# Optimization experiments

Hardware: AMD Instinct MI355X
Metric: run time of the kernel (lower is better)

The kernel has to match this reference:

```python
import math
import jax, jax.numpy as jnp
import numpy as np

B, T, C, H = 2, 2048, 1024, 16
MAX_SEQ = 2048


def _make_pe(max_seq: int, dim: int, base: float = 10000.0) -> np.ndarray:
    pe = np.zeros((max_seq, dim), dtype=np.float32)
    position = np.arange(max_seq, dtype=np.float32)[:, None]
    div_term = np.exp(np.arange(0, dim, 2, dtype=np.float32) * (-math.log(base) / dim))
    pe[:, 0::2] = np.sin(position * div_term)
    pe[:, 1::2] = np.cos(position * div_term)
    return pe


def setup_inputs() -> dict:
    key = jax.random.key(0)
    k1, k2, k3 = jax.random.split(key, 3)
    x = jax.random.normal(k1, (B, T, C), dtype=jnp.float32)
    # torch Linear default init scale ~ 1/sqrt(fan_in)
    w_qkv = jax.random.normal(k2, (3 * C, C), dtype=jnp.float32) / math.sqrt(C)
    w_proj = jax.random.normal(k3, (C, C), dtype=jnp.float32) / math.sqrt(C)
    pe = jnp.asarray(_make_pe(MAX_SEQ, C))
    return {"x": x, "w_qkv": w_qkv, "w_proj": w_proj, "pe": pe}


def reference(x, w_qkv, w_proj, pe):
    b, t, c = x.shape
    h = H
    d = c // h
    # RoPE module adds sinusoidal PE under torch.no_grad() -> stop_gradient
    xp = jax.lax.stop_gradient(x + pe[None, :t, :])
    qkv = xp @ w_qkv.T  # [b, t, 3c]
    q, k, v = jnp.split(qkv, 3, axis=-1)
    q = q.reshape(b, t, h, d).transpose(0, 2, 1, 3)  # bhtd
    k = k.reshape(b, t, h, d).transpose(0, 2, 1, 3)
    v = v.reshape(b, t, h, d).transpose(0, 2, 1, 3)
    att = jnp.einsum("bhqd,bhkd->bhqk", q, k) * (1.0 / math.sqrt(d))
    causal = jnp.tril(jnp.ones((t, t), dtype=bool))  # [t, t]
    att = jnp.where(causal[None, None], att, -jnp.inf)
    att = jax.nn.softmax(att, axis=-1)
    y = jnp.einsum("bhqk,bhkd->bhqd", att, v)
    y = y.transpose(0, 2, 1, 3).reshape(b, t, c)
    return y @ w_proj.T
```

## Files before the change

kernel.cpp:

```cpp
#include <hip/hip_runtime.h>
#include <cstdint>

typedef __bf16 bf16x8 __attribute__((ext_vector_type(8)));
typedef __bf16 bf16x4 __attribute__((ext_vector_type(4)));
typedef float  f32x4  __attribute__((ext_vector_type(4)));

static constexpr int kB = 2, kT = 2048, kC = 1024, kH = 16, kD = 64;
static constexpr int kK = 1024;

__device__ __forceinline__ uint16_t f2bf(float f) {
  uint32_t u = __builtin_bit_cast(uint32_t, f);
  u += 0x7FFFu + ((u >> 16) & 1u);
  return (uint16_t)(u >> 16);
}

__device__ __forceinline__ void gl_lds16(const void* g, void* l) {
  __builtin_amdgcn_global_load_lds((__attribute__((address_space(1))) void*)(void*)g,
                                   (__attribute__((address_space(3))) void*)l, 16, 0, 0);
}

__global__ __launch_bounds__(256) void prep_all(const float* __restrict__ x,
                                                const float* __restrict__ pe,
                                                const float* __restrict__ wqkv,
                                                const float* __restrict__ wproj,
                                                uint16_t* __restrict__ xp,
                                                uint16_t* __restrict__ wq,
                                                uint16_t* __restrict__ wp) {
  constexpr int NX = kB * kT * kC / 4;
  constexpr int NWQ = 3 * kC * kC / 4;
  const int i = blockIdx.x * 256 + threadIdx.x;
  if (i < NX) {
    const float4 xv = ((const float4*)x)[i];
    const int c4 = i & (kC / 4 - 1);
    const int t = (i / (kC / 4)) & (kT - 1);
    const float4 pv = ((const float4*)pe)[t * (kC / 4) + c4];
    ushort4 o;
    o.x = f2bf(xv.x + pv.x);
    o.y = f2bf(xv.y + pv.y);
    o.z = f2bf(xv.z + pv.z);
    o.w = f2bf(xv.w + pv.w);
    ((ushort4*)xp)[i] = o;
  } else if (i < NX + NWQ) {
    const int j = i - NX;
    const float4 v = ((const float4*)wqkv)[j];
    ushort4 u;
    u.x = f2bf(v.x); u.y = f2bf(v.y); u.z = f2bf(v.z); u.w = f2bf(v.w);
    ((ushort4*)wq)[j] = u;
  } else {
    const int j = i - NX - NWQ;
    const float4 v = ((const float4*)wproj)[j];
    ushort4 u;
    u.x = f2bf(v.x); u.y = f2bf(v.y); u.z = f2bf(v.z); u.w = f2bf(v.w);
    ((ushort4*)wp)[j] = u;
  }
}

__global__ __launch_bounds__(512, 2) void gemm_qkv(const uint16_t* __restrict__ A,
                                                   const uint16_t* __restrict__ W,
                                                   uint16_t* __restrict__ qb,
                                                   uint16_t* __restrict__ kb,
                                                   uint16_t* __restrict__ vT) {
  __shared__ __align__(1024) char lds[131072];
  const int tid = threadIdx.x;
  const int lane = tid & 63;
  const int wid = tid >> 6;
  const int l15 = lane & 15, l4 = lane >> 4;
  const int WM = wid >> 2, WN = wid & 3;
  const int orig = (int)blockIdx.x;
  const int xcd = orig & 7, j = orig >> 3;
  const int m0 = (xcd * 2 + (j & 1)) * 256;
  const int n0 = (j >> 1) * 256;

  f32x4 acc[2][4][4] = {};
  bf16x8 bfp[2][4];

  auto stage = [&](int isA, int buf, int kt) {
#pragma unroll
    for (int c = 0; c < 4; ++c) {
      const int off = (c * 512 + tid) * 16;
      const int lr = off >> 7, cbl = off & 127;
      const size_t grow = (size_t)((isA ? m0 : n0) + lr) * kK + kt * 64;
      gl_lds16((const char*)(isA ? A : W) + grow * 2 + (cbl ^ ((lr & 7) << 4)),
               lds + (isA ? 0 : 65536) + buf * 32768 + off);
    }
  };

#define QKV_PHASE(CBUF, H, SA, SBUF, KT, VM)                                      \
  {                                                                               \
    stage(SA, SBUF, KT);                                                          \
    if (VM == 4)                                                                  \
      asm volatile("s_waitcnt vmcnt(4)" ::: "memory");                            \
    else                                                                          \
      asm volatile("s_waitcnt vmcnt(8)" ::: "memory");                            \
    __builtin_amdgcn_s_barrier();                                                 \
    asm volatile("" ::: "memory");                                                \
    const char* Ab = lds + (CBUF)*32768;                                          \
    const char* Bb = lds + 65536 + (CBUF)*32768;                                  \
    if ((H) == 0) {                                                               \
      _Pragma("unroll") for (int ks = 0; ks < 2; ++ks)                            \
          _Pragma("unroll") for (int nt = 0; nt < 4; ++nt) {                      \
        const int lr = WN * 64 + nt * 16 + l15;                                   \
        bfp[ks][nt] = *(const bf16x8*)(Bb + lr * 128 +                            \
                                       ((ks * 64 + l4 * 16) ^ ((lr & 7) << 4)));  \
      }                                                                           \
    }                                                                             \
    _Pragma("unroll") for (int ks = 0; ks < 2; ++ks) {                            \
      bf16x8 af[4];                                                               \
      _Pragma("unroll") for (int mt = 0; mt < 4; ++mt) {                          \
        const int lr = (H)*128 + WM * 64 + mt * 16 + l15;                         \
        af[mt] = *(const bf16x8*)(Ab + lr * 128 +                                 \
                                  ((ks * 64 + l4 * 16) ^ ((lr & 7) << 4)));       \
      }                                                                           \
      __builtin_amdgcn_s_setprio(1);                                              \
      _Pragma("unroll") for (int mt = 0; mt < 4; ++mt)                            \
          _Pragma("unroll") for (int nt = 0; nt < 4; ++nt)                        \
              acc[H][mt][nt] = __builtin_amdgcn_mfma_f32_16x16x32_bf16(           \
                  af[mt], bfp[ks][nt], acc[H][mt][nt], 0, 0, 0);                  \
      __builtin_amdgcn_s_setprio(0);                                              \
    }                                                                             \
    asm volatile("" ::: "memory");                                                \
    __builtin_amdgcn_s_barrier();                                                 \
    asm volatile("" ::: "memory");                                                \
  }

  stage(1, 0, 0);
  stage(0, 0, 0);

  for (int i = 0; i < 8; ++i) {
    const int ktb1 = 2 * i + 1;
    const int ktb0 = (2 * i + 2 > 15) ? 15 : 2 * i + 2;
    QKV_PHASE(0, 0, 1, 1, ktb1, 4);
    QKV_PHASE(0, 1, 0, 1, ktb1, 8);
    QKV_PHASE(1, 0, 1, 0, ktb0, 4);
    QKV_PHASE(1, 1, 0, 0, ktb0, 8);
  }
  asm volatile("s_waitcnt vmcnt(0)" ::: "memory");
  __builtin_amdgcn_s_barrier();
  asm volatile("" ::: "memory");

  const int sec = n0 >> 10;
  const int b = m0 >> 11, tb = m0 & (kT - 1);
  if (sec < 2) {
    uint16_t* dst = (sec == 0) ? qb : kb;
#pragma unroll
    for (int h = 0; h < 2; ++h)
#pragma unroll
      for (int mt = 0; mt < 4; ++mt)
#pragma unroll
        for (int nt = 0; nt < 4; ++nt)
#pragma unroll
          for (int r = 0; r < 4; ++r) {
            const int m = h * 128 + WM * 64 + mt * 16 + l4 * 4 + r;
            const int nn = (n0 & (kC - 1)) + WN * 64 + nt * 16 + l15;
            const int hh = nn >> 6, d = nn & 63;
            dst[((size_t)((b * kH + hh) * kT + tb + m)) * kD + d] =
                f2bf(acc[h][mt][nt][r]);
          }
  } else {
#pragma unroll
    for (int h = 0; h < 2; ++h)
#pragma unroll
      for (int mt = 0; mt < 4; ++mt)
#pragma unroll
        for (int nt = 0; nt < 4; ++nt) {
          const int nl = WN * 64 + nt * 16 + l15;
          const int mb2 = (h * 128 + WM * 64 + mt * 16 + l4 * 4) * 2;
          ushort4 pk;
          pk.x = f2bf(acc[h][mt][nt][0]);
          pk.y = f2bf(acc[h][mt][nt][1]);
          pk.z = f2bf(acc[h][mt][nt][2]);
          pk.w = f2bf(acc[h][mt][nt][3]);
          *(ushort4*)(lds + nl * 512 + (mb2 ^ ((nl & 7) << 4))) = pk;
        }
    asm volatile("" ::: "memory");
    __builtin_amdgcn_s_barrier();
    asm volatile("" ::: "memory");
#pragma unroll
    for (int it = 0; it < 16; ++it) {
      const int chunk = it * 512 + tid;
      const int nr = chunk >> 5, mb = (chunk & 31) * 16;
      const bf16x8 v = *(const bf16x8*)(lds + nr * 512 + (mb ^ ((nr & 7) << 4)));
      const int nn = (n0 - 2048) + nr;
      const int hh = nn >> 6, d = nn & 63;
      *(bf16x8*)(vT + ((size_t)((b * kH + hh) * kD + d)) * kT + tb + (chunk & 31) * 8) = v;
    }
  }
#undef QKV_PHASE
}

__global__ __launch_bounds__(256) void gemm_proj(const uint16_t* __restrict__ A,
                                                 const uint16_t* __restrict__ W,
                                                 float* __restrict__ out) {
  __shared__ __align__(1024) char lds[32768];
  const int lane = threadIdx.x & 63;
  const int wid = threadIdx.x >> 6;
  const int l15 = lane & 15, l4 = lane >> 4;
  const int wm = wid >> 1, wn = wid & 1;
  const int orig = (int)(blockIdx.y * gridDim.x + blockIdx.x);
  const int xcd = orig & 7, j = orig >> 3;
  const int m0 = (xcd * 4 + (j & 3)) * 128;
  const int n0 = (j >> 2) * 128;

  f32x4 acc[4][4] = {};

  for (int k0 = 0; k0 < kK; k0 += 64) {
#pragma unroll
    for (int jj = 0; jj < 4; ++jj) {
      const int off = wid * 4096 + jj * 1024 + lane * 16;
      const int row = off >> 7;
      const int colb = (off & 127) ^ ((row & 7) << 4);
      gl_lds16((const char*)A + ((size_t)(m0 + row) * kK + k0) * 2 + colb,
               lds + wid * 4096 + jj * 1024);
      gl_lds16((const char*)W + ((size_t)(n0 + row) * kK + k0) * 2 + colb,
               lds + 16384 + wid * 4096 + jj * 1024);
    }
    __syncthreads();
#pragma unroll
    for (int ks = 0; ks < 2; ++ks) {
      bf16x8 af[4], bf_[4];
#pragma unroll
      for (int mt = 0; mt < 4; ++mt) {
        const int r = wm * 64 + mt * 16 + l15;
        const int cb = (l4 * 16 + ks * 64) ^ ((r & 7) << 4);
        af[mt] = *(const bf16x8*)(lds + r * 128 + cb);
      }
#pragma unroll
      for (int nt = 0; nt < 4; ++nt) {
        const int r = wn * 64 + nt * 16 + l15;
        const int cb = (l4 * 16 + ks * 64) ^ ((r & 7) << 4);
        bf_[nt] = *(const bf16x8*)(lds + 16384 + r * 128 + cb);
      }
#pragma unroll
      for (int mt = 0; mt < 4; ++mt)
#pragma unroll
        for (int nt = 0; nt < 4; ++nt)
          acc[mt][nt] = __builtin_amdgcn_mfma_f32_16x16x32_bf16(af[mt], bf_[nt],
                                                                acc[mt][nt], 0, 0, 0);
    }
    __syncthreads();
  }

#pragma unroll
  for (int mt = 0; mt < 4; ++mt)
#pragma unroll
    for (int nt = 0; nt < 4; ++nt)
#pragma unroll
      for (int r = 0; r < 4; ++r) {
        const int m = m0 + wm * 64 + mt * 16 + l4 * 4 + r;
        const int n = n0 + wn * 64 + nt * 16 + l15;
        out[(size_t)m * kC + n] = acc[mt][nt][r];
      }
}

__global__ __launch_bounds__(256, 4) void attn(const uint16_t* __restrict__ qb,
                                               const uint16_t* __restrict__ kb,
                                               const uint16_t* __restrict__ vT,
                                               uint16_t* __restrict__ y) {
  __shared__ __align__(1024) char lds[40960];
  const int lane = threadIdx.x & 63;
  const int wid = threadIdx.x >> 6;
  const int l15 = lane & 15, l4 = lane >> 4;
  const int bh = blockIdx.x;
  const int qt = (int)(gridDim.y - 1) - (int)blockIdx.y;
  const int q0 = qt * 64 + wid * 16;
  const size_t base = (size_t)bh * kT * kD;
  const uint16_t* Q = qb + base;
  const uint16_t* Kp = kb + base;
  const uint16_t* Vt = vT + base;
  char* P = lds + 32768 + wid * 2048;
  const int xr = (l15 & 7) << 4;

  bf16x8 qf[2];
#pragma unroll
  for (int ks = 0; ks < 2; ++ks) {
    bf16x8 t = *(const bf16x8*)(Q + (size_t)(q0 + l15) * kD + ks * 32 + l4 * 8);
#pragma unroll
    for (int i = 0; i < 8; ++i) t[i] = (__bf16)((float)t[i] * 0.1803368801f);
    qf[ks] = t;
  }
  bf16x8 ones;
#pragma unroll
  for (int i = 0; i < 8; ++i) ones[i] = (__bf16)1.0f;

  float m_ = -1e30f;
  f32x4 o[4];
  f32x4 ol = {0.f, 0.f, 0.f, 0.f};
#pragma unroll
  for (int nt = 0; nt < 4; ++nt) o[nt] = (f32x4){0.f, 0.f, 0.f, 0.f};

  const int nkt = qt + 1;

  auto STAGE = [&](int bi, int k0) {
#pragma unroll
    for (int c = 0; c < 2; ++c) {
      const int call = wid * 2 + c;
      const int row = call * 8 + (lane >> 3);
      const int colb = (((lane & 7) ^ ((lane >> 3) & 7)) << 4);
      gl_lds16((const char*)Kp + ((size_t)(k0 + row) * kD) * 2 + colb,
               lds + bi * 8192 + call * 1024);
      gl_lds16((const char*)Vt + ((size_t)row * kT + k0) * 2 + colb,
               lds + 16384 + bi * 8192 + call * 1024);
    }
  };

  int cur = 0;
  STAGE(0, 0);
  for (int kt = 0; kt < nkt; ++kt) {
    const int k0 = kt * 64;
    const bool hasnext = (kt + 1 < nkt);
    if (hasnext) STAGE(cur ^ 1, k0 + 64);
    if (hasnext)
      asm volatile("s_waitcnt vmcnt(4)" ::: "memory");
    else
      asm volatile("s_waitcnt vmcnt(0)" ::: "memory");
    __builtin_amdgcn_s_barrier();
    asm volatile("" ::: "memory");

    const char* Kb = lds + cur * 8192;
    const char* Vb = lds + 16384 + cur * 8192;

    f32x4 s[4] = {};
    __builtin_amdgcn_s_setprio(1);
#pragma unroll
    for (int ks = 0; ks < 2; ++ks)
#pragma unroll
      for (int nt = 0; nt < 4; ++nt) {
        const bf16x8 kf =
            *(const bf16x8*)(Kb + (nt * 16 + l15) * 128 + ((ks * 64 + l4 * 16) ^ xr));
        s[nt] = __builtin_amdgcn_mfma_f32_16x16x32_bf16(kf, qf[ks], s[nt], 0, 0, 0);
      }
    __builtin_amdgcn_s_setprio(0);

    if (kt == nkt - 1) {
      const int qq = q0 + l15;
#pragma unroll
      for (int nt = 0; nt < 4; ++nt)
#pragma unroll
        for (int r = 0; r < 4; ++r)
          if (k0 + nt * 16 + l4 * 4 + r > qq) s[nt][r] = -1e30f;
    }

    float pm = s[0][0];
#pragma unroll
    for (int nt = 0; nt < 4; ++nt)
#pragma unroll
      for (int r = 0; r < 4; ++r) pm = fmaxf(pm, s[nt][r]);
    if (!__all(pm <= m_ + 11.0f)) {
      float rm = fmaxf(pm, __shfl_xor(pm, 16));
      rm = fmaxf(rm, __shfl_xor(rm, 32));
      const float newm = fmaxf(m_, rm);
      const float sc = exp2f(m_ - newm);
      m_ = newm;
#pragma unroll
      for (int nt = 0; nt < 4; ++nt)
#pragma unroll
        for (int r = 0; r < 4; ++r) o[nt][r] *= sc;
#pragma unroll
      for (int r = 0; r < 4; ++r) ol[r] *= sc;
    }
#pragma unroll
    for (int nt = 0; nt < 4; ++nt)
#pragma unroll
      for (int r = 0; r < 4; ++r) s[nt][r] = exp2f(s[nt][r] - m_);

#pragma unroll
    for (int nt = 0; nt < 4; ++nt) {
      bf16x4 pk;
#pragma unroll
      for (int r = 0; r < 4; ++r) pk[r] = (__bf16)s[nt][r];
      *(bf16x4*)(P + l15 * 128 + ((nt * 32 + l4 * 8) ^ xr)) = pk;
    }
    asm volatile("s_waitcnt lgkmcnt(0)" ::: "memory");
    __builtin_amdgcn_sched_barrier(0);

    bf16x8 pf[2];
#pragma unroll
    for (int ks = 0; ks < 2; ++ks)
      pf[ks] = *(const bf16x8*)(P + l15 * 128 + ((ks * 64 + l4 * 16) ^ xr));
    __builtin_amdgcn_s_setprio(1);
#pragma unroll
    for (int ks = 0; ks < 2; ++ks) {
#pragma unroll
      for (int nt = 0; nt < 4; ++nt) {
        const bf16x8 vf =
            *(const bf16x8*)(Vb + (nt * 16 + l15) * 128 + ((ks * 64 + l4 * 16) ^ xr));
        o[nt] = __builtin_amdgcn_mfma_f32_16x16x32_bf16(vf, pf[ks], o[nt], 0, 0, 0);
      }
      ol = __builtin_amdgcn_mfma_f32_16x16x32_bf16(ones, pf[ks], ol, 0, 0, 0);
    }
    __builtin_amdgcn_s_setprio(0);

    __builtin_amdgcn_s_barrier();
    asm volatile("" ::: "memory");
    cur ^= 1;
  }

  const float inv = 1.0f / ol[0];
  const int b = bh >> 4, h = bh & 15;
  const int q = q0 + l15;
#pragma unroll
  for (int nt = 0; nt < 4; ++nt) {
    bf16x4 yv;
#pragma unroll
    for (int r = 0; r < 4; ++r) yv[r] = (__bf16)(o[nt][r] * inv);
    *(bf16x4*)(y + ((size_t)(b * kT + q)) * kC + h * kD + nt * 16 + l4 * 4) = yv;
  }
}

extern "C" void kernel_launch(void* const* d_in, const int* in_sizes, int n_in,
                              void* d_out, int out_size, void* d_ws, size_t ws_size,
                              hipStream_t stream) {
  const float* x = (const float*)d_in[0];
  const float* wqkv = (const float*)d_in[1];
  const float* wproj = (const float*)d_in[2];
  const float* pe = (const float*)d_in[3];

  char* ws = (char*)d_ws;
  uint16_t* xp = (uint16_t*)(ws);
  uint16_t* wq = (uint16_t*)(ws + (size_t)(8u << 20));
  uint16_t* wp = (uint16_t*)(ws + (size_t)(14u << 20));
  uint16_t* qbuf = (uint16_t*)(ws + (size_t)(16u << 20));
  uint16_t* kbuf = (uint16_t*)(ws + (size_t)(24u << 20));
  uint16_t* vTb = (uint16_t*)(ws + (size_t)(32u << 20));

  prep_all<<<dim3(8192), 256, 0, stream>>>(x, pe, wqkv, wproj, xp, wq, wp);

  gemm_qkv<<<dim3(192), 512, 0, stream>>>(xp, wq, qbuf, kbuf, vTb);

  attn<<<dim3(kB * kH, kT / 64), 256, 0, stream>>>(qbuf, kbuf, vTb, xp);

  gemm_proj<<<dim3(32, 8), 256, 0, stream>>>(xp, wp, (float*)d_out);
}
```

Baseline: 108.0 us.

## Retile QKV GEMM to 256x192 for full CU occupancy; pipeline projection GEMM

The QKV GEMM changes from 256x256 to 256x192 tiles, so the grid grows from 192 to 256 blocks and fills all 256 CUs. Because a 192-wide tile can straddle the Q/K/V sections, the epilogue now picks the destination per element and writes vT with scattered strided stores, dropping the LDS transpose path. The projection GEMM is rewritten to use the same double-buffered, split-phase pipelined structure with waitcnt-based overlap. The risks are poorer coalescing of the vT stores and higher register use in the new proj kernel.

Measured after the change: 113.9 us. 5.5% more time.

```diff
diff --git a/kernel.cpp b/kernel.cpp
--- a/kernel.cpp
+++ b/kernel.cpp
@@ -60,7 +60,7 @@
                                                    uint16_t* __restrict__ qb,
                                                    uint16_t* __restrict__ kb,
                                                    uint16_t* __restrict__ vT) {
-  __shared__ __align__(1024) char lds[131072];
+  __shared__ __align__(1024) char lds[114688];
   const int tid = threadIdx.x;
   const int lane = tid & 63;
   const int wid = tid >> 6;
@@ -69,37 +69,47 @@
   const int orig = (int)blockIdx.x;
   const int xcd = orig & 7, j = orig >> 3;
   const int m0 = (xcd * 2 + (j & 1)) * 256;
-  const int n0 = (j >> 1) * 256;
-
-  f32x4 acc[2][4][4] = {};
-  bf16x8 bfp[2][4];
-
-  auto stage = [&](int isA, int buf, int kt) {
+  const int n0 = (j >> 1) * 192;
+
+  f32x4 acc[2][4][3] = {};
+  bf16x8 bfp[2][3];
+
+  auto stageA = [&](int buf, int kt) {
 #pragma unroll
     for (int c = 0; c < 4; ++c) {
       const int off = (c * 512 + tid) * 16;
       const int lr = off >> 7, cbl = off & 127;
-      const size_t grow = (size_t)((isA ? m0 : n0) + lr) * kK + kt * 64;
-      gl_lds16((const char*)(isA ? A : W) + grow * 2 + (cbl ^ ((lr & 7) << 4)),
-               lds + (isA ? 0 : 65536) + buf * 32768 + off);
+      gl_lds16((const char*)A + ((size_t)(m0 + lr) * kK + kt * 64) * 2 +
+                   (cbl ^ ((lr & 7) << 4)),
+               lds + buf * 32768 + off);
+    }
+  };
+  auto stageB = [&](int buf, int kt) {
+#pragma unroll
+    for (int c = 0; c < 3; ++c) {
+      const int off = (c * 512 + tid) * 16;
+      const int lr = off >> 7, cbl = off & 127;
+      gl_lds16((const char*)W + ((size_t)(n0 + lr) * kK + kt * 64) * 2 +
+                   (cbl ^ ((lr & 7) << 4)),
+               lds + 65536 + buf * 24576 + off);
     }
   };
 
 #define QKV_PHASE(CBUF, H, SA, SBUF, KT, VM)                                      \
   {                                                                               \
-    stage(SA, SBUF, KT);                                                          \
+    if (SA) stageA(SBUF, KT); else stageB(SBUF, KT);                              \
     if (VM == 4)                                                                  \
       asm volatile("s_waitcnt vmcnt(4)" ::: "memory");                            \
     else                                                                          \
-      asm volatile("s_waitcnt vmcnt(8)" ::: "memory");                            \
+      asm volatile("s_waitcnt vmcnt(7)" ::: "memory");                            \
     __builtin_amdgcn_s_barrier();                                                 \
     asm volatile("" ::: "memory");                                                \
     const char* Ab = lds + (CBUF)*32768;                                          \
-    const char* Bb = lds + 65536 + (CBUF)*32768;                                  \
+    const char* Bb = lds + 65536 + (CBUF)*24576;                                  \
     if ((H) == 0) {                                                               \
       _Pragma("unroll") for (int ks = 0; ks < 2; ++ks)                            \
-          _Pragma("unroll") for (int nt = 0; nt < 4; ++nt) {                      \
-        const int lr = WN * 64 + nt * 16 + l15;                                   \
+          _Pragma("unroll") for (int nt = 0; nt < 3; ++nt) {                      \
+        const int lr = WN * 48 + nt * 16 + l15;                                   \
         bfp[ks][nt] = *(const bf16x8*)(Bb + lr * 128 +                            \
                                        ((ks * 64 + l4 * 16) ^ ((lr & 7) << 4)));  \
       }                                                                           \
@@ -113,6 +123,112 @@
       }                                                                           \
       __builtin_amdgcn_s_setprio(1);                                              \
       _Pragma("unroll") for (int mt = 0; mt < 4; ++mt)                            \
+          _Pragma("unroll") for (int nt = 0; nt < 3; ++nt)                        \
+              acc[H][mt][nt] = __builtin_amdgcn_mfma_f32_16x16x32_bf16(           \
+                  af[mt], bfp[ks][nt], acc[H][mt][nt], 0, 0, 0);                  \
+      __builtin_amdgcn_s_setprio(0);                                              \
+    }                                                                             \
+    asm volatile("" ::: "memory");                                                \
+    __builtin_amdgcn_s_barrier();                                                 \
+    asm volatile("" ::: "memory");                                                \
+  }
+
+  stageA(0, 0);
+  stageB(0, 0);
+
+  for (int i = 0; i < 8; ++i) {
+    const int ktb1 = 2 * i + 1;
+    const int ktb0 = (2 * i + 2 > 15) ? 15 : 2 * i + 2;
+    QKV_PHASE(0, 0, 1, 1, ktb1, 4);
+    QKV_PHASE(0, 1, 0, 1, ktb1, 7);
+    QKV_PHASE(1, 0, 1, 0, ktb0, 4);
+    QKV_PHASE(1, 1, 0, 0, ktb0, 7);
+  }
+  asm volatile("s_waitcnt vmcnt(0)" ::: "memory");
+  __builtin_amdgcn_s_barrier();
+  asm volatile("" ::: "memory");
+
+  const int b = m0 >> 11, tb = m0 & (kT - 1);
+#pragma unroll
+  for (int h = 0; h < 2; ++h)
+#pragma unroll
+    for (int mt = 0; mt < 4; ++mt)
+#pragma unroll
+      for (int nt = 0; nt < 3; ++nt)
+#pragma unroll
+        for (int r = 0; r < 4; ++r) {
+          const int m = h * 128 + WM * 64 + mt * 16 + l4 * 4 + r;
+          const int t = tb + m;
+          const int n = n0 + WN * 48 + nt * 16 + l15;
+          const int sec = n >> 10, nn = n & (kC - 1);
+          const int hh = nn >> 6, d = nn & 63;
+          const uint16_t v = f2bf(acc[h][mt][nt][r]);
+          if (sec == 0)
+            qb[((size_t)((b * kH + hh) * kT + t)) * kD + d] = v;
+          else if (sec == 1)
+            kb[((size_t)((b * kH + hh) * kT + t)) * kD + d] = v;
+          else
+            vT[((size_t)((b * kH + hh) * kD + d)) * kT + t] = v;
+        }
+#undef QKV_PHASE
+}
+
+__global__ __launch_bounds__(256, 2) void gemm_proj(const uint16_t* __restrict__ A,
+                                                    const uint16_t* __restrict__ W,
+                                                    float* __restrict__ out) {
+  __shared__ __align__(1024) char lds[65536];
+  const int tid = threadIdx.x;
+  const int lane = tid & 63;
+  const int wid = tid >> 6;
+  const int l15 = lane & 15, l4 = lane >> 4;
+  const int WM = wid >> 1, WN = wid & 1;
+  const int orig = (int)blockIdx.x;
+  const int xcd = orig & 7, j = orig >> 3;
+  const int m0 = (xcd * 4 + (j & 3)) * 128;
+  const int n0 = (j >> 2) * 128;
+
+  f32x4 acc[2][2][4] = {};
+  bf16x8 bfp[2][4];
+
+  auto stage = [&](int isA, int buf, int kt) {
+#pragma unroll
+    for (int c = 0; c < 4; ++c) {
+      const int off = (c * 256 + tid) * 16;
+      const int lr = off >> 7, cbl = off & 127;
+      const size_t grow = (size_t)((isA ? m0 : n0) + lr) * kK + kt * 64;
+      gl_lds16((const char*)(isA ? A : W) + grow * 2 + (cbl ^ ((lr & 7) << 4)),
+               lds + (isA ? 0 : 32768) + buf * 16384 + off);
+    }
+  };
+
+#define PRJ_PHASE(CBUF, H, SA, SBUF, KT, VM)                                      \
+  {                                                                               \
+    stage(SA, SBUF, KT);                                                          \
+    if (VM == 4)                                                                  \
+      asm volatile("s_waitcnt vmcnt(4)" ::: "memory");                            \
+    else                                                                          \
+      asm volatile("s_waitcnt vmcnt(8)" ::: "memory");                            \
+    __builtin_amdgcn_s_barrier();                                                 \
+    asm volatile("" ::: "memory");                                                \
+    const char* Ab = lds + (CBUF)*16384;                                          \
+    const char* Bb = lds + 32768 + (CBUF)*16384;                                  \
+    if ((H) == 0) {                                                               \
+      _Pragma("unroll") for (int ks = 0; ks < 2; ++ks)                            \
+          _Pragma("unroll") for (int nt = 0; nt < 4; ++nt) {                      \
+        const int lr = WN * 64 + nt * 16 + l15;                                   \
+        bfp[ks][nt] = *(const bf16x8*)(Bb + lr * 128 +                            \
+                                       ((ks * 64 + l4 * 16) ^ ((lr & 7) << 4)));  \
+      }                                                                           \
+    }                                                                             \
+    _Pragma("unroll") for (int ks = 0; ks < 2; ++ks) {                            \
+      bf16x8 af[2];                                                               \
+      _Pragma("unroll") for (int mt = 0; mt < 2; ++mt) {                          \
+        const int lr = (H)*64 + WM * 32 + mt * 16 + l15;                          \
+        af[mt] = *(const bf16x8*)(Ab + lr * 128 +                                 \
+                                  ((ks * 64 + l4 * 16) ^ ((lr & 7) << 4)));       \
+      }                                                                           \
+      __builtin_amdgcn_s_setprio(1);                                              \
+      _Pragma("unroll") for (int mt = 0; mt < 2; ++mt)                            \
           _Pragma("unroll") for (int nt = 0; nt < 4; ++nt)                        \
               acc[H][mt][nt] = __builtin_amdgcn_mfma_f32_16x16x32_bf16(           \
                   af[mt], bfp[ks][nt], acc[H][mt][nt], 0, 0, 0);                  \
@@ -129,127 +245,28 @@
   for (int i = 0; i < 8; ++i) {
     const int ktb1 = 2 * i + 1;
     const int ktb0 = (2 * i + 2 > 15) ? 15 : 2 * i + 2;
-    QKV_PHASE(0, 0, 1, 1, ktb1, 4);
-    QKV_PHASE(0, 1, 0, 1, ktb1, 8);
-    QKV_PHASE(1, 0, 1, 0, ktb0, 4);
-    QKV_PHASE(1, 1, 0, 0, ktb0, 8);
+    PRJ_PHASE(0, 0, 1, 1, ktb1, 4);
+    PRJ_PHASE(0, 1, 0, 1, ktb1, 8);
+    PRJ_PHASE(1, 0, 1, 0, ktb0, 4);
+    PRJ_PHASE(1, 1, 0, 0, ktb0, 8);
   }
   asm volatile("s_waitcnt vmcnt(0)" ::: "memory");
   __builtin_amdgcn_s_barrier();
   asm volatile("" ::: "memory");
 
-  const int sec = n0 >> 10;
-  const int b = m0 >> 11, tb = m0 & (kT - 1);
-  if (sec < 2) {
-    uint16_t* dst = (sec == 0) ? qb : kb;
-#pragma unroll
-    for (int h = 0; h < 2; ++h)
-#pragma unroll
-      for (int mt = 0; mt < 4; ++mt)
-#pragma unroll
-        for (int nt = 0; nt < 4; ++nt)
-#pragma unroll
-          for (int r = 0; r < 4; ++r) {
-            const int m = h * 128 + WM * 64 + mt * 16 + l4 * 4 + r;
-            const int nn = (n0 & (kC - 1)) + WN * 64 + nt * 16 + l15;
-            const int hh = nn >> 6, d = nn & 63;
-            dst[((size_t)((b * kH + hh) * kT + tb + m)) * kD + d] =
-                f2bf(acc[h][mt][nt][r]);
-          }
-  } else {
-#pragma unroll
-    for (int h = 0; h < 2; ++h)
-#pragma unroll
-      for (int mt = 0; mt < 4; ++mt)
-#pragma unroll
-        for (int nt = 0; nt < 4; ++nt) {
-          const int nl = WN * 64 + nt * 16 + l15;
-          const int mb2 = (h * 128 + WM * 64 + mt * 16 + l4 * 4) * 2;
-          ushort4 pk;
-          pk.x = f2bf(acc[h][mt][nt][0]);
-          pk.y = f2bf(acc[h][mt][nt][1]);
-          pk.z = f2bf(acc[h][mt][nt][2]);
-          pk.w = f2bf(acc[h][mt][nt][3]);
-          *(ushort4*)(lds + nl * 512 + (mb2 ^ ((nl & 7) << 4))) = pk;
+#pragma unroll
+  for (int h = 0; h < 2; ++h)
+#pragma unroll
+    for (int mt = 0; mt < 2; ++mt)
+#pragma unroll
+      for (int nt = 0; nt < 4; ++nt)
+#pragma unroll
+        for (int r = 0; r < 4; ++r) {
+          const int m = m0 + h * 64 + WM * 32 + mt * 16 + l4 * 4 + r;
+          const int n = n0 + WN * 64 + nt * 16 + l15;
+          out[(size_t)m * kC + n] = acc[h][mt][nt][r];
         }
-    asm volatile("" ::: "memory");
-    __builtin_amdgcn_s_barrier();
-    asm volatile("" ::: "memory");
-#pragma unroll
-    for (int it = 0; it < 16; ++it) {
-      const int chunk = it * 512 + tid;
-      const int nr = chunk >> 5, mb = (chunk & 31) * 16;
-      const bf16x8 v = *(const bf16x8*)(lds + nr * 512 + (mb ^ ((nr & 7) << 4)));
-      const int nn = (n0 - 2048) + nr;
-      const int hh = nn >> 6, d = nn & 63;
-      *(bf16x8*)(vT + ((size_t)((b * kH + hh) * kD + d)) * kT + tb + (chunk & 31) * 8) = v;
-    }
-  }
-#undef QKV_PHASE
-}
-
-__global__ __launch_bounds__(256) void gemm_proj(const uint16_t* __restrict__ A,
-                                                 const uint16_t* __restrict__ W,
-                                                 float* __restrict__ out) {
-  __shared__ __align__(1024) char lds[32768];
-  const int lane = threadIdx.x & 63;
-  const int wid = threadIdx.x >> 6;
-  const int l15 = lane & 15, l4 = lane >> 4;
-  const int wm = wid >> 1, wn = wid & 1;
-  const int orig = (int)(blockIdx.y * gridDim.x + blockIdx.x);
-  const int xcd = orig & 7, j = orig >> 3;
-  const int m0 = (xcd * 4 + (j & 3)) * 128;
-  const int n0 = (j >> 2) * 128;
-
-  f32x4 acc[4][4] = {};
-
-  for (int k0 = 0; k0 < kK; k0 += 64) {
-#pragma unroll
-    for (int jj = 0; jj < 4; ++jj) {
-      const int off = wid * 4096 + jj * 1024 + lane * 16;
-      const int row = off >> 7;
-      const int colb = (off & 127) ^ ((row & 7) << 4);
-      gl_lds16((const char*)A + ((size_t)(m0 + row) * kK + k0) * 2 + colb,
-               lds + wid * 4096 + jj * 1024);
-      gl_lds16((const char*)W + ((size_t)(n0 + row) * kK + k0) * 2 + colb,
-               lds + 16384 + wid * 4096 + jj * 1024);
-    }
-    __syncthreads();
-#pragma unroll
-    for (int ks = 0; ks < 2; ++ks) {
-      bf16x8 af[4], bf_[4];
-#pragma unroll
-      for (int mt = 0; mt < 4; ++mt) {
-        const int r = wm * 64 + mt * 16 + l15;
-        const int cb = (l4 * 16 + ks * 64) ^ ((r & 7) << 4);
-        af[mt] = *(const bf16x8*)(lds + r * 128 + cb);
-      }
-#pragma unroll
-      for (int nt = 0; nt < 4; ++nt) {
-        const int r = wn * 64 + nt * 16 + l15;
-        const int cb = (l4 * 16 + ks * 64) ^ ((r & 7) << 4);
-        bf_[nt] = *(const bf16x8*)(lds + 16384 + r * 128 + cb);
-      }
-#pragma unroll
-      for (int mt = 0; mt < 4; ++mt)
-#pragma unroll
-        for (int nt = 0; nt < 4; ++nt)
-          acc[mt][nt] = __builtin_amdgcn_mfma_f32_16x16x32_bf16(af[mt], bf_[nt],
-                                                                acc[mt][nt], 0, 0, 0);
-    }
-    __syncthreads();
-  }
-
-#pragma unroll
-  for (int mt = 0; mt < 4; ++mt)
-#pragma unroll
-    for (int nt = 0; nt < 4; ++nt)
-#pragma unroll
-      for (int r = 0; r < 4; ++r) {
-        const int m = m0 + wm * 64 + mt * 16 + l4 * 4 + r;
-        const int n = n0 + wn * 64 + nt * 16 + l15;
-        out[(size_t)m * kC + n] = acc[mt][nt][r];
-      }
+#undef PRJ_PHASE
 }
 
 __global__ __launch_bounds__(256, 4) void attn(const uint16_t* __restrict__ qb,
@@ -425,9 +442,9 @@
 
   prep_all<<<dim3(8192), 256, 0, stream>>>(x, pe, wqkv, wproj, xp, wq, wp);
 
-  gemm_qkv<<<dim3(192), 512, 0, stream>>>(xp, wq, qbuf, kbuf, vTb);
+  gemm_qkv<<<dim3(256), 512, 0, stream>>>(xp, wq, qbuf, kbuf, vTb);
 
   attn<<<dim3(kB * kH, kT / 64), 256, 0, stream>>>(qbuf, kbuf, vTb, xp);
 
-  gemm_proj<<<dim3(32, 8), 256, 0, stream>>>(xp, wp, (float*)d_out);
-}
+  gemm_proj<<<dim3(256), 256, 0, stream>>>(xp, wp, (float*)d_out);
+}
```
